# Kernel optimization log

Hardware: AMD Instinct MI355X
Metric: run time of the kernel (lower is better)

## Reference

```python
import jax, jax.numpy as jnp
import numpy as np

B, N, DIM = 2, 2048, 1024
HEADS, DIM_HEAD = 16, 64
INNER = HEADS * DIM_HEAD  # 1024
SCALE = DIM_HEAD ** -0.5


def setup_inputs() -> dict:
    key = jax.random.key(0)
    ks = jax.random.split(key, 8)
    s = DIM ** -0.5
    return {
        "x1": jax.random.normal(ks[0], (B, N, DIM), jnp.float32),
        "x2": jax.random.normal(ks[1], (B, N, DIM), jnp.float32),
        "W_qkv1": jax.random.normal(ks[2], (DIM, INNER * 3), jnp.float32) * s,
        "W_qkv2": jax.random.normal(ks[3], (DIM, INNER * 3), jnp.float32) * s,
        "W_out1": jax.random.normal(ks[4], (INNER, DIM), jnp.float32) * s,
        "b_out1": jnp.zeros((DIM,), jnp.float32),
        "W_out2": jax.random.normal(ks[5], (INNER, DIM), jnp.float32) * s,
        "b_out2": jnp.zeros((DIM,), jnp.float32),
    }


def _split_heads(t):
    # [b, n, (h d)] -> [b, h, n, d]
    b, n, _ = t.shape
    return t.reshape(b, n, HEADS, DIM_HEAD).transpose(0, 2, 1, 3)


def _merge_heads(t):
    # [b, h, n, d] -> [b, n, (h d)]
    b, h, n, d = t.shape
    return t.transpose(0, 2, 1, 3).reshape(b, n, h * d)


def reference(x1, x2, W_qkv1, W_qkv2, W_out1, b_out1, W_out2, b_out2):
    qkv1 = x1 @ W_qkv1  # [b, n, 3*inner]
    qkv2 = x2 @ W_qkv2
    q1, k1, v1 = [_split_heads(t) for t in jnp.split(qkv1, 3, axis=-1)]
    q2, k2, v2 = [_split_heads(t) for t in jnp.split(qkv2, 3, axis=-1)]

    # direction 1: queries from stream 2 attend to keys/values of stream 1
    dots1 = jnp.einsum('bhid,bhjd->bhij', q2, k1) * SCALE
    attn1 = jax.nn.softmax(dots1, axis=-1)
    out1 = jnp.einsum('bhij,bhjd->bhid', attn1, v1)
    out1 = _merge_heads(out1) @ W_out1 + b_out1

    # direction 2: queries from stream 1 attend to keys/values of stream 2
    dots2 = jnp.einsum('bhid,bhjd->bhij', q1, k2) * SCALE
    attn2 = jax.nn.softmax(dots2, axis=-1)
    out2 = jnp.einsum('bhij,bhjd->bhid', attn2, v2)
    out2 = _merge_heads(out2) @ W_out2 + b_out2

    return (out1, out2)
```

## Files before the change

### kernel.cpp

```cpp
#include <hip/hip_runtime.h>
#include <cmath>

typedef __attribute__((ext_vector_type(8))) short short8;
typedef __attribute__((ext_vector_type(4))) float f32x4;
typedef __attribute__((ext_vector_type(16))) float f32x16;
using u16 = unsigned short;

#define DEV static __device__ __forceinline__

DEV u16 f2bf(float f) {
  union { float f; unsigned u; } v; v.f = f;
  unsigned r = v.u + 0x7FFFu + ((v.u >> 16) & 1u);
  return (u16)(r >> 16);
}

DEV unsigned cvtpk(float lo, float hi_) {
  unsigned d;
  asm("v_cvt_pk_bf16_f32 %0, %1, %2" : "=v"(d) : "v"(lo), "v"(hi_));
  return d;
}

DEV void gld16(const void* g, void* l) {
  __builtin_amdgcn_global_load_lds(
      (const __attribute__((address_space(1))) unsigned*)g,
      (__attribute__((address_space(3))) unsigned*)l, 16, 0, 0);
}

__global__ void probe_scale(float* out) {
  if (threadIdx.x == 0 && blockIdx.x == 0) {
    float b = __builtin_amdgcn_exp2f(1.0f);
    out[0] = 0.125f / logf(b);
    out[1] = (fabsf(b - 2.0f) < 1e-3f) ? 0.0f : 1.0f;
  }
}

__global__ __launch_bounds__(256) void conv_f32_bf16(const float* __restrict__ s0,
                                                     const float* __restrict__ s1,
                                                     u16* __restrict__ d0,
                                                     u16* __restrict__ d1, int n8) {
  const float* src = blockIdx.z ? s1 : s0;
  u16* dst = blockIdx.z ? d1 : d0;
  int i = blockIdx.x * 256 + threadIdx.x;
  if (i >= n8) return;
  const float4* s = reinterpret_cast<const float4*>(src) + (size_t)i * 2;
  float4 a = s[0], b = s[1];
  union { u16 s[8]; uint4 v; } t;
  t.s[0]=f2bf(a.x); t.s[1]=f2bf(a.y); t.s[2]=f2bf(a.z); t.s[3]=f2bf(a.w);
  t.s[4]=f2bf(b.x); t.s[5]=f2bf(b.y); t.s[6]=f2bf(b.z); t.s[7]=f2bf(b.w);
  reinterpret_cast<uint4*>(dst)[i] = t.v;
}

__global__ __launch_bounds__(256) void transpose_w(const float* __restrict__ s0,
                                                   const float* __restrict__ s1,
                                                   u16* __restrict__ d0,
                                                   u16* __restrict__ d1, int R, int C,
                                                   int qcols,
                                                   const float* __restrict__ qscale_p) {
  const float* src = blockIdx.z ? s1 : s0;
  u16* dst = blockIdx.z ? d1 : d0;
  const float qscale = qscale_p ? qscale_p[0] : 1.0f;
  __shared__ float tile[32][33];
  int tx = threadIdx.x & 31, ty = threadIdx.x >> 5;
  int rb = blockIdx.y * 32, cb = blockIdx.x * 32;
#pragma unroll
  for (int j = 0; j < 32; j += 8)
    tile[ty + j][tx] = src[(size_t)(rb + ty + j) * C + cb + tx];
  __syncthreads();
#pragma unroll
  for (int j = 0; j < 32; j += 8) {
    int c = cb + ty + j;
    float sc = (c < qcols) ? qscale : 1.0f;
    dst[(size_t)c * R + rb + tx] = f2bf(tile[tx][ty + j] * sc);
  }
}

extern __shared__ char dsmem[];

__global__ __launch_bounds__(512, 2) void gemm256(
    const u16* __restrict__ A0, const u16* __restrict__ A1,
    const u16* __restrict__ B0, const u16* __restrict__ B1,
    u16* __restrict__ Q0, u16* __restrict__ Q1,
    u16* __restrict__ V0, u16* __restrict__ V1) {
  const int orig = blockIdx.x;
  const int wgid = (orig & 7) * 48 + (orig >> 3);
  const int z = wgid / 192, rr_ = wgid % 192;
  const int bx = rr_ / 12, by = rr_ % 12;
  const u16* Ag = z ? A1 : A0;
  const u16* Bg = z ? B1 : B0;
  const size_t m0 = (size_t)bx * 256, n0 = (size_t)by * 256;
  const int K = 1024;

  const int tid = threadIdx.x;
  const int lane = tid & 63;
  const int wave = tid >> 6;
  const int wm = wave >> 2, wn = wave & 3;
  const int lr = lane & 15, lk = lane >> 4;

  f32x4 acc[8][4] = {};

  auto STG = [&](int buf, int kt, int opi) {
    int idx = opi * 512 + tid;
    char* base = dsmem + buf * 65536;
    if (idx < 2048) {
      int r = idx >> 3, c = idx & 7;
      gld16(Ag + (m0 + r) * (size_t)K + kt * 64 + ((c ^ (r & 7)) * 8), base + idx * 16);
    } else {
      int j = idx - 2048;
      int r = j >> 3, c = j & 7;
      gld16(Bg + (n0 + r) * (size_t)K + kt * 64 + ((c ^ (r & 7)) * 8), base + 32768 + j * 16);
    }
  };
  auto DSA = [&](short8* af, int buf, int mg, int kh) {
#pragma unroll
    for (int i = 0; i < 4; ++i) {
      int row = wm * 128 + (mg * 4 + i) * 16 + lr;
      af[i] = *reinterpret_cast<const short8*>(
          dsmem + buf * 65536 + row * 128 + (((kh * 4 + lk) ^ (row & 7)) * 16));
    }
  };
  auto DSB = [&](short8* bf_, int buf, int kh) {
#pragma unroll
    for (int j = 0; j < 4; ++j) {
      int row = wn * 64 + j * 16 + lr;
      bf_[j] = *reinterpret_cast<const short8*>(
          dsmem + buf * 65536 + 32768 + row * 128 + (((kh * 4 + lk) ^ (row & 7)) * 16));
    }
  };

#pragma unroll
  for (int o = 0; o < 8; ++o) STG(0, 0, o);
  asm volatile("s_waitcnt vmcnt(0)" ::: "memory");
  __syncthreads();

  int cur = 0;
  for (int kt = 0; kt < 16; ++kt) {
    short8 af[4], bf_[4];
    const int more = (kt < 15);

    DSA(af, cur, 0, 0); DSB(bf_, cur, 0);
    if (more) { STG(cur ^ 1, kt + 1, 0); STG(cur ^ 1, kt + 1, 1);
                STG(cur ^ 1, kt + 1, 2); STG(cur ^ 1, kt + 1, 3); }
    __builtin_amdgcn_s_barrier();
    asm volatile("s_waitcnt lgkmcnt(0)" ::: "memory");
    __builtin_amdgcn_sched_barrier(0);
    __builtin_amdgcn_s_setprio(1);
#pragma unroll
    for (int i = 0; i < 4; ++i)
#pragma unroll
      for (int j = 0; j < 4; ++j)
        acc[i][j] = __builtin_amdgcn_mfma_f32_16x16x32_bf16(af[i], bf_[j], acc[i][j], 0, 0, 0);
    __builtin_amdgcn_s_setprio(0);
    __builtin_amdgcn_s_barrier();

    DSA(af, cur, 1, 0);
    if (more) { STG(cur ^ 1, kt + 1, 4); STG(cur ^ 1, kt + 1, 5);
                STG(cur ^ 1, kt + 1, 6); STG(cur ^ 1, kt + 1, 7); }
    __builtin_amdgcn_s_barrier();
    asm volatile("s_waitcnt lgkmcnt(0)" ::: "memory");
    __builtin_amdgcn_sched_barrier(0);
    __builtin_amdgcn_s_setprio(1);
#pragma unroll
    for (int i = 0; i < 4; ++i)
#pragma unroll
      for (int j = 0; j < 4; ++j)
        acc[4 + i][j] = __builtin_amdgcn_mfma_f32_16x16x32_bf16(af[i], bf_[j], acc[4 + i][j], 0, 0, 0);
    __builtin_amdgcn_s_setprio(0);
    __builtin_amdgcn_s_barrier();

    DSA(af, cur, 0, 1); DSB(bf_, cur, 1);
    __builtin_amdgcn_s_barrier();
    asm volatile("s_waitcnt lgkmcnt(0)" ::: "memory");
    __builtin_amdgcn_sched_barrier(0);
    __builtin_amdgcn_s_setprio(1);
#pragma unroll
    for (int i = 0; i < 4; ++i)
#pragma unroll
      for (int j = 0; j < 4; ++j)
        acc[i][j] = __builtin_amdgcn_mfma_f32_16x16x32_bf16(af[i], bf_[j], acc[i][j], 0, 0, 0);
    __builtin_amdgcn_s_setprio(0);
    __builtin_amdgcn_s_barrier();

    DSA(af, cur, 1, 1);
    __builtin_amdgcn_s_barrier();
    asm volatile("s_waitcnt lgkmcnt(0)" ::: "memory");
    __builtin_amdgcn_sched_barrier(0);
    __builtin_amdgcn_s_setprio(1);
#pragma unroll
    for (int i = 0; i < 4; ++i)
#pragma unroll
      for (int j = 0; j < 4; ++j)
        acc[4 + i][j] = __builtin_amdgcn_mfma_f32_16x16x32_bf16(af[i], bf_[j], acc[4 + i][j], 0, 0, 0);
    __builtin_amdgcn_s_setprio(0);
    asm volatile("s_waitcnt vmcnt(0)" ::: "memory");
    __builtin_amdgcn_s_barrier();
    cur ^= 1;
  }

  const int row0 = (int)m0 + wm * 128;
  const int col0 = (int)n0 + wn * 64;
  u16* Qo = z ? Q1 : Q0;
  u16* Vo = z ? V1 : V0;
  if (col0 < 2048) {
#pragma unroll
    for (int mf = 0; mf < 8; ++mf)
#pragma unroll
      for (int nf = 0; nf < 4; ++nf) {
        int col = col0 + nf * 16 + lr;
#pragma unroll
        for (int g = 0; g < 4; ++g) {
          int row = row0 + mf * 16 + lk * 4 + g;
          Qo[(size_t)row * 3072 + col] = f2bf(acc[mf][nf][g]);
        }
      }
  } else {
#pragma unroll
    for (int mf = 0; mf < 8; ++mf)
#pragma unroll
      for (int nf = 0; nf < 4; ++nf) {
        int col = col0 + nf * 16 + lr;
        int row = row0 + mf * 16 + lk * 4;
        size_t vbase = ((size_t)((row >> 11) * 1024 + (col - 2048))) * 2048 + (row & 2047);
        union { u16 s[4]; unsigned long long v; } pk;
#pragma unroll
        for (int g = 0; g < 4; ++g) pk.s[g] = f2bf(acc[mf][nf][g]);
        *reinterpret_cast<unsigned long long*>(Vo + vbase) = pk.v;
      }
  }
}

__global__ __launch_bounds__(256) void gemm_bt(
    const u16* __restrict__ A0, const u16* __restrict__ A1,
    const u16* __restrict__ B0, const u16* __restrict__ B1,
    float* __restrict__ Cf0, float* __restrict__ Cf1,
    const float* __restrict__ bias0, const float* __restrict__ bias1,
    int M, int N, int K) {
  const int z = blockIdx.z;
  const u16* A  = z ? A1 : A0;
  const u16* Bt = z ? B1 : B0;
  float* Cf = z ? Cf1 : Cf0;
  const float* bias = z ? bias1 : bias0;

  __shared__ __align__(16) char smem[32768];
  char* As = smem;
  char* Bs = smem + 16384;
  const int tid = threadIdx.x;
  const int lane = tid & 63, wave = tid >> 6;
  const int wm = wave >> 1, wn = wave & 1;
  const int lr = lane & 15, lk = lane >> 4;
  const size_t m0 = (size_t)blockIdx.x * 128, n0 = (size_t)blockIdx.y * 128;

  f32x4 acc[4][4] = {};

  for (int k0 = 0; k0 < K; k0 += 64) {
    __syncthreads();
#pragma unroll
    for (int i = 0; i < 4; ++i) {
      int idx = tid + i * 256;
      int r = idx >> 3, c = idx & 7;
      int cs = c ^ (r & 7);
      gld16(A + (m0 + r) * (size_t)K + k0 + cs * 8, As + idx * 16);
    }
#pragma unroll
    for (int i = 0; i < 4; ++i) {
      int idx = tid + i * 256;
      int r = idx >> 3, c = idx & 7;
      int cs = c ^ (r & 7);
      gld16(Bt + (n0 + r) * (size_t)K + k0 + cs * 8, Bs + idx * 16);
    }
    __syncthreads();
#pragma unroll
    for (int kk = 0; kk < 2; ++kk) {
      short8 af[4], bfr[4];
#pragma unroll
      for (int mf = 0; mf < 4; ++mf) {
        int r = wm * 64 + mf * 16 + lr;
        af[mf] = *reinterpret_cast<const short8*>(As + r * 128 + (((kk * 4 + lk) ^ (r & 7)) * 16));
      }
#pragma unroll
      for (int nf = 0; nf < 4; ++nf) {
        int r = wn * 64 + nf * 16 + lr;
        bfr[nf] = *reinterpret_cast<const short8*>(Bs + r * 128 + (((kk * 4 + lk) ^ (r & 7)) * 16));
      }
#pragma unroll
      for (int mf = 0; mf < 4; ++mf)
#pragma unroll
        for (int nf = 0; nf < 4; ++nf)
          acc[mf][nf] = __builtin_amdgcn_mfma_f32_16x16x32_bf16(af[mf], bfr[nf], acc[mf][nf], 0, 0, 0);
    }
  }
  const int row0 = (int)m0 + wm * 64, col0 = (int)n0 + wn * 64;
#pragma unroll
  for (int nf = 0; nf < 4; ++nf) {
    int col = col0 + nf * 16 + lr;
    float bv = bias[col];
#pragma unroll
    for (int mf = 0; mf < 4; ++mf)
#pragma unroll
      for (int g = 0; g < 4; ++g) {
        int row = row0 + mf * 16 + lk * 4 + g;
        Cf[(size_t)row * N + col] = acc[mf][nf][g] + bv;
      }
  }
}

#define KOFF0 0
#define VOFF0 (8192 + 64)
#define KOFF1 (16384 + 128)
#define VOFF1 (KOFF1 + 8192 + 64)

__global__ __launch_bounds__(256, 2) void flash(
    const u16* __restrict__ qkv1, const u16* __restrict__ qkv2,
    const u16* __restrict__ vT1, const u16* __restrict__ vT2,
    u16* __restrict__ ao1, u16* __restrict__ ao2,
    const float* __restrict__ sflag) {
  const int bid = blockIdx.x;
  const int bh_dir = bid & 63;
  const int qt = bid >> 6;
  const int dir = bh_dir >> 5;
  const int bh = bh_dir & 31;
  const int b = bh >> 4, h = bh & 15;
  const u16* qkvQ  = dir ? qkv1 : qkv2;
  const u16* qkvKV = dir ? qkv2 : qkv1;
  const u16* vT    = dir ? vT2 : vT1;
  u16* Oout        = dir ? ao2 : ao1;

  const bool nat = (sflag[1] != 0.0f);

  __shared__ __align__(16) char smem[33024];

  const int tid = threadIdx.x;
  const int lane = tid & 63, wave = tid >> 6;
  const int l31 = lane & 31, hi = lane >> 5;

  const int qbase = qt * 256 + wave * 64;
  const u16* qp0 = qkvQ + (size_t)(b * 2048 + qbase + l31) * 3072 + h * 64 + hi * 8;
  const u16* qp1 = qp0 + (size_t)32 * 3072;
  short8 qf0[4], qf1[4];
#pragma unroll
  for (int c = 0; c < 4; ++c) {
    qf0[c] = *reinterpret_cast<const short8*>(qp0 + c * 16);
    qf1[c] = *reinterpret_cast<const short8*>(qp1 + c * 16);
  }

  auto STAGE = [&](char* kb, char* vb, int kv0) {
#pragma unroll
    for (int i = 0; i < 2; ++i) {
      int idx = tid + i * 256;
      int r = idx >> 3, c = idx & 7, cs = c ^ (r & 7);
      gld16(qkvKV + (size_t)(b * 2048 + kv0 + r) * 3072 + 1024 + h * 64 + cs * 8, kb + idx * 16);
      gld16(vT + (size_t)(bh * 64 + r) * 2048 + kv0 + cs * 8, vb + idx * 16);
    }
  };

  auto EXPV = [&](f32x16& S) {
    if (nat) {
#pragma unroll
      for (int r = 0; r < 16; ++r) S[r] = __builtin_amdgcn_exp2f(S[r]);
    } else {
#pragma unroll
      for (int r = 0; r < 16; ++r) S[r] = __builtin_exp2f(S[r]);
    }
  };

  short8 ones;
#pragma unroll
  for (int j = 0; j < 8; ++j) ones[j] = (short)0x3F80;

  f32x16 oA0 = {}, oA1 = {}, oB0 = {}, oB1 = {}, laccA = {}, laccB = {};

  STAGE(smem + KOFF0, smem + VOFF0, 0);

  union U8 { unsigned u[4]; short8 s8; };

  for (int t = 0; t < 32; ++t) {
    char* Ks = smem + ((t & 1) ? KOFF1 : KOFF0);
    char* Vs = smem + ((t & 1) ? VOFF1 : VOFF0);
    __syncthreads();
    if (t < 31)
      STAGE(smem + ((t & 1) ? KOFF0 : KOFF1), smem + ((t & 1) ? VOFF0 : VOFF1), (t + 1) * 64);

    short8 kf[8];
#pragma unroll
    for (int c = 0; c < 4; ++c) {
      int sw = ((c * 2 + hi) ^ (l31 & 7)) * 16;
      kf[c]     = *reinterpret_cast<const short8*>(Ks + l31 * 128 + sw);
      kf[c + 4] = *reinterpret_cast<const short8*>(Ks + (32 + l31) * 128 + sw);
    }

    f32x16 sA0 = {}, sA1 = {};
#pragma unroll
    for (int c = 0; c < 4; ++c) {
      sA0 = __builtin_amdgcn_mfma_f32_32x32x16_bf16(kf[c],     qf0[c], sA0, 0, 0, 0);
      sA1 = __builtin_amdgcn_mfma_f32_32x32x16_bf16(kf[c + 4], qf0[c], sA1, 0, 0, 0);
    }
    EXPV(sA0); EXPV(sA1);
    short8 paA[4];
#pragma unroll
    for (int kc = 0; kc < 4; ++kc) {
      const f32x16& S = (kc < 2) ? sA0 : sA1;
      int rb = (kc & 1) * 8;
      unsigned a0 = cvtpk(S[rb + 0], S[rb + 1]);
      unsigned b0 = cvtpk(S[rb + 4], S[rb + 5]);
      asm volatile("v_permlane32_swap_b32 %0, %1" : "+v"(a0), "+v"(b0));
      unsigned a1 = cvtpk(S[rb + 2], S[rb + 3]);
      unsigned b1 = cvtpk(S[rb + 6], S[rb + 7]);
      asm volatile("v_permlane32_swap_b32 %0, %1" : "+v"(a1), "+v"(b1));
      U8 u; u.u[0] = a0; u.u[1] = a1; u.u[2] = b0; u.u[3] = b1;
      paA[kc] = u.s8;
    }

    f32x16 sB0 = {}, sB1 = {};
#pragma unroll
    for (int c = 0; c < 4; ++c) {
      sB0 = __builtin_amdgcn_mfma_f32_32x32x16_bf16(kf[c],     qf1[c], sB0, 0, 0, 0);
      sB1 = __builtin_amdgcn_mfma_f32_32x32x16_bf16(kf[c + 4], qf1[c], sB1, 0, 0, 0);
    }

    short8 vf[8];
#pragma unroll
    for (int kc = 0; kc < 4; ++kc) {
      int sw = ((kc * 2 + hi) ^ (l31 & 7)) * 16;
      vf[kc]     = *reinterpret_cast<const short8*>(Vs + l31 * 128 + sw);
      vf[kc + 4] = *reinterpret_cast<const short8*>(Vs + (32 + l31) * 128 + sw);
    }

    EXPV(sB0); EXPV(sB1);
    short8 paB[4];
#pragma unroll
    for (int kc = 0; kc < 4; ++kc) {
      const f32x16& S = (kc < 2) ? sB0 : sB1;
      int rb = (kc & 1) * 8;
      unsigned a0 = cvtpk(S[rb + 0], S[rb + 1]);
      unsigned b0 = cvtpk(S[rb + 4], S[rb + 5]);
      asm volatile("v_permlane32_swap_b32 %0, %1" : "+v"(a0), "+v"(b0));
      unsigned a1 = cvtpk(S[rb + 2], S[rb + 3]);
      unsigned b1 = cvtpk(S[rb + 6], S[rb + 7]);
      asm volatile("v_permlane32_swap_b32 %0, %1" : "+v"(a1), "+v"(b1));
      U8 u; u.u[0] = a0; u.u[1] = a1; u.u[2] = b0; u.u[3] = b1;
      paB[kc] = u.s8;
    }

#pragma unroll
    for (int kc = 0; kc < 4; ++kc) {
      oA0 = __builtin_amdgcn_mfma_f32_32x32x16_bf16(paA[kc], vf[kc],     oA0, 0, 0, 0);
      oA1 = __builtin_amdgcn_mfma_f32_32x32x16_bf16(paA[kc], vf[kc + 4], oA1, 0, 0, 0);
      oB0 = __builtin_amdgcn_mfma_f32_32x32x16_bf16(paB[kc], vf[kc],     oB0, 0, 0, 0);
      oB1 = __builtin_amdgcn_mfma_f32_32x32x16_bf16(paB[kc], vf[kc + 4], oB1, 0, 0, 0);
      laccA = __builtin_amdgcn_mfma_f32_32x32x16_bf16(paA[kc], ones, laccA, 0, 0, 0);
      laccB = __builtin_amdgcn_mfma_f32_32x32x16_bf16(paB[kc], ones, laccB, 0, 0, 0);
    }
  }

  const int rowbase = b * 2048 + qt * 256 + wave * 64;
#pragma unroll
  for (int r = 0; r < 16; ++r) {
    int q = (r & 3) + 8 * (r >> 2) + 4 * hi;
    float liA = 1.0f / laccA[r], liB = 1.0f / laccB[r];
    u16* opA = Oout + (size_t)(rowbase + q) * 1024 + h * 64 + l31;
    u16* opB = opA + (size_t)32 * 1024;
    opA[0]  = f2bf(oA0[r] * liA);
    opA[32] = f2bf(oA1[r] * liA);
    opB[0]  = f2bf(oB0[r] * liB);
    opB[32] = f2bf(oB1[r] * liB);
  }
}

extern "C" void kernel_launch(void* const* d_in, const int* in_sizes, int n_in,
                              void* d_out, int out_size, void* d_ws, size_t ws_size,
                              hipStream_t stream) {
  const float* x1  = (const float*)d_in[0];
  const float* x2  = (const float*)d_in[1];
  const float* Wq1 = (const float*)d_in[2];
  const float* Wq2 = (const float*)d_in[3];
  const float* Wo1 = (const float*)d_in[4];
  const float* bo1 = (const float*)d_in[5];
  const float* Wo2 = (const float*)d_in[6];
  const float* bo2 = (const float*)d_in[7];
  float* out = (float*)d_out;

  char* ws = (char*)d_ws;
  u16* x1b  = (u16*)(ws + 0);
  u16* x2b  = (u16*)(ws + 8388608);
  u16* Wq1t = (u16*)(ws + 16777216);
  u16* Wq2t = (u16*)(ws + 23068672);
  u16* Wo1t = (u16*)(ws + 29360128);
  u16* Wo2t = (u16*)(ws + 31457280);
  u16* qkv1 = (u16*)(ws + 33554432);
  u16* qkv2 = (u16*)(ws + 58720256);
  u16* vT1  = (u16*)(ws + 83886080);
  u16* vT2  = (u16*)(ws + 92274688);
  u16* ao1  = (u16*)(ws + 100663296);
  u16* ao2  = (u16*)(ws + 109051904);

  float* scale_buf = (float*)(qkv1 + 2048);

  hipFuncSetAttribute(reinterpret_cast<const void*>(gemm256),
                      hipFuncAttributeMaxDynamicSharedMemorySize, 131072);

  probe_scale<<<dim3(1), 64, 0, stream>>>(scale_buf);

  conv_f32_bf16<<<dim3(2048, 1, 2), 256, 0, stream>>>(x1, x2, x1b, x2b, 4194304 / 8);
  transpose_w<<<dim3(96, 32, 2), 256, 0, stream>>>(Wq1, Wq2, Wq1t, Wq2t, 1024, 3072,
                                                   1024, scale_buf);
  transpose_w<<<dim3(32, 32, 2), 256, 0, stream>>>(Wo1, Wo2, Wo1t, Wo2t, 1024, 1024,
                                                   0, nullptr);

  gemm256<<<dim3(384), 512, 131072, stream>>>(x1b, x2b, Wq1t, Wq2t,
                                              qkv1, qkv2, vT1, vT2);

  flash<<<dim3(512), 256, 0, stream>>>(qkv1, qkv2, vT1, vT2, ao1, ao2, scale_buf);

  gemm_bt<<<dim3(32, 8, 2), 256, 0, stream>>>(ao1, ao2, Wo1t, Wo2t,
                                              out, out + 4194304, bo1, bo2,
                                              4096, 1024, 1024);
}
```

Baseline: 214.5 us.

## Shrink QKV GEMM tile to 256x128 and use inline-asm hardware exp

The QKV projection GEMM now uses 256x128 output tiles with a 4x2 wave grid instead of 256x256. That doubles the grid to 768 workgroups and lowers LDS use to 96KB per block, so more blocks are resident and the 304 CUs are loaded more evenly. The cost is less data reuse per tile and more global traffic for the A operand. Separately, the flash kernel's exp now calls v_exp_f32 through inline asm, and the probe kernel checks its accuracy more carefully and falls back to the natural-exp scale if the check fails. The asm volatile exp may also limit how the compiler schedules the exp instructions.

```diff
diff --git a/kernel.cpp b/kernel.cpp
--- a/kernel.cpp
+++ b/kernel.cpp
@@ -26,11 +26,29 @@
       (__attribute__((address_space(3))) unsigned*)l, 16, 0, 0);
 }
 
+DEV float hw_exp(float x) {
+  float y;
+  asm volatile("v_exp_f32 %0, %1\n\ts_nop 1" : "=v"(y) : "v"(x));
+  return y;
+}
+
 __global__ void probe_scale(float* out) {
   if (threadIdx.x == 0 && blockIdx.x == 0) {
-    float b = __builtin_amdgcn_exp2f(1.0f);
-    out[0] = 0.125f / logf(b);
-    out[1] = (fabsf(b - 2.0f) < 1e-3f) ? 0.0f : 1.0f;
+    float one;
+    asm volatile("v_mov_b32 %0, 1.0" : "=v"(one));
+    float b = hw_exp(one);
+    float lnb = logf(b);
+    bool ok = (fabsf(b - 2.0f) < 0.25f) && (lnb > 0.1f);
+    const float xs[3] = {0.3333f, -5.7f, 9.1f};
+    for (int i = 0; i < 3; ++i) {
+      float xo;
+      asm volatile("v_mov_b32 %0, %1" : "=v"(xo) : "v"(xs[i]));
+      float yn = hw_exp(xo);
+      float yr = expf(lnb * xs[i]);
+      ok = ok && (fabsf(yn - yr) <= 2e-4f * fabsf(yr));
+    }
+    out[0] = ok ? (0.125f / lnb) : (0.125f / 0.69314718056f);
+    out[1] = ok ? 1.0f : 0.0f;
   }
 }
 
@@ -82,25 +100,25 @@
     u16* __restrict__ Q0, u16* __restrict__ Q1,
     u16* __restrict__ V0, u16* __restrict__ V1) {
   const int orig = blockIdx.x;
-  const int wgid = (orig & 7) * 48 + (orig >> 3);
-  const int z = wgid / 192, rr_ = wgid % 192;
-  const int bx = rr_ / 12, by = rr_ % 12;
+  const int wgid = (orig & 7) * 96 + (orig >> 3);
+  const int z = wgid / 384, rr_ = wgid % 384;
+  const int bx = rr_ / 24, by = rr_ % 24;
   const u16* Ag = z ? A1 : A0;
   const u16* Bg = z ? B1 : B0;
-  const size_t m0 = (size_t)bx * 256, n0 = (size_t)by * 256;
+  const size_t m0 = (size_t)bx * 256, n0 = (size_t)by * 128;
   const int K = 1024;
 
   const int tid = threadIdx.x;
   const int lane = tid & 63;
   const int wave = tid >> 6;
-  const int wm = wave >> 2, wn = wave & 3;
+  const int wm = wave >> 1, wn = wave & 1;
   const int lr = lane & 15, lk = lane >> 4;
 
-  f32x4 acc[8][4] = {};
+  f32x4 acc[4][4] = {};
 
   auto STG = [&](int buf, int kt, int opi) {
     int idx = opi * 512 + tid;
-    char* base = dsmem + buf * 65536;
+    char* base = dsmem + buf * 49152;
     if (idx < 2048) {
       int r = idx >> 3, c = idx & 7;
       gld16(Ag + (m0 + r) * (size_t)K + kt * 64 + ((c ^ (r & 7)) * 8), base + idx * 16);
@@ -110,12 +128,12 @@
       gld16(Bg + (n0 + r) * (size_t)K + kt * 64 + ((c ^ (r & 7)) * 8), base + 32768 + j * 16);
     }
   };
-  auto DSA = [&](short8* af, int buf, int mg, int kh) {
+  auto DSA = [&](short8* af, int buf, int kh) {
 #pragma unroll
     for (int i = 0; i < 4; ++i) {
-      int row = wm * 128 + (mg * 4 + i) * 16 + lr;
+      int row = wm * 64 + i * 16 + lr;
       af[i] = *reinterpret_cast<const short8*>(
-          dsmem + buf * 65536 + row * 128 + (((kh * 4 + lk) ^ (row & 7)) * 16));
+          dsmem + buf * 49152 + row * 128 + (((kh * 4 + lk) ^ (row & 7)) * 16));
     }
   };
   auto DSB = [&](short8* bf_, int buf, int kh) {
@@ -123,12 +141,12 @@
     for (int j = 0; j < 4; ++j) {
       int row = wn * 64 + j * 16 + lr;
       bf_[j] = *reinterpret_cast<const short8*>(
-          dsmem + buf * 65536 + 32768 + row * 128 + (((kh * 4 + lk) ^ (row & 7)) * 16));
+          dsmem + buf * 49152 + 32768 + row * 128 + (((kh * 4 + lk) ^ (row & 7)) * 16));
     }
   };
 
 #pragma unroll
-  for (int o = 0; o < 8; ++o) STG(0, 0, o);
+  for (int o = 0; o < 6; ++o) STG(0, 0, o);
   asm volatile("s_waitcnt vmcnt(0)" ::: "memory");
   __syncthreads();
 
@@ -137,9 +155,9 @@
     short8 af[4], bf_[4];
     const int more = (kt < 15);
 
-    DSA(af, cur, 0, 0); DSB(bf_, cur, 0);
-    if (more) { STG(cur ^ 1, kt + 1, 0); STG(cur ^ 1, kt + 1, 1);
-                STG(cur ^ 1, kt + 1, 2); STG(cur ^ 1, kt + 1, 3); }
+    DSA(af, cur, 0); DSB(bf_, cur, 0);
+    if (more) { STG(cur ^ 1, kt + 1, 0); STG(cur ^ 1, kt + 1, 1); STG(cur ^ 1, kt + 1, 2);
+                STG(cur ^ 1, kt + 1, 3); STG(cur ^ 1, kt + 1, 4); STG(cur ^ 1, kt + 1, 5); }
     __builtin_amdgcn_s_barrier();
     asm volatile("s_waitcnt lgkmcnt(0)" ::: "memory");
     __builtin_amdgcn_sched_barrier(0);
@@ -152,9 +170,7 @@
     __builtin_amdgcn_s_setprio(0);
     __builtin_amdgcn_s_barrier();
 
-    DSA(af, cur, 1, 0);
-    if (more) { STG(cur ^ 1, kt + 1, 4); STG(cur ^ 1, kt + 1, 5);
-                STG(cur ^ 1, kt + 1, 6); STG(cur ^ 1, kt + 1, 7); }
+    DSA(af, cur, 1); DSB(bf_, cur, 1);
     __builtin_amdgcn_s_barrier();
     asm volatile("s_waitcnt lgkmcnt(0)" ::: "memory");
     __builtin_amdgcn_sched_barrier(0);
@@ -163,46 +179,20 @@
     for (int i = 0; i < 4; ++i)
 #pragma unroll
       for (int j = 0; j < 4; ++j)
-        acc[4 + i][j] = __builtin_amdgcn_mfma_f32_16x16x32_bf16(af[i], bf_[j], acc[4 + i][j], 0, 0, 0);
-    __builtin_amdgcn_s_setprio(0);
-    __builtin_amdgcn_s_barrier();
-
-    DSA(af, cur, 0, 1); DSB(bf_, cur, 1);
-    __builtin_amdgcn_s_barrier();
-    asm volatile("s_waitcnt lgkmcnt(0)" ::: "memory");
-    __builtin_amdgcn_sched_barrier(0);
-    __builtin_amdgcn_s_setprio(1);
-#pragma unroll
-    for (int i = 0; i < 4; ++i)
-#pragma unroll
-      for (int j = 0; j < 4; ++j)
         acc[i][j] = __builtin_amdgcn_mfma_f32_16x16x32_bf16(af[i], bf_[j], acc[i][j], 0, 0, 0);
-    __builtin_amdgcn_s_setprio(0);
-    __builtin_amdgcn_s_barrier();
-
-    DSA(af, cur, 1, 1);
-    __builtin_amdgcn_s_barrier();
-    asm volatile("s_waitcnt lgkmcnt(0)" ::: "memory");
-    __builtin_amdgcn_sched_barrier(0);
-    __builtin_amdgcn_s_setprio(1);
-#pragma unroll
-    for (int i = 0; i < 4; ++i)
-#pragma unroll
-      for (int j = 0; j < 4; ++j)
-        acc[4 + i][j] = __builtin_amdgcn_mfma_f32_16x16x32_bf16(af[i], bf_[j], acc[4 + i][j], 0, 0, 0);
     __builtin_amdgcn_s_setprio(0);
     asm volatile("s_waitcnt vmcnt(0)" ::: "memory");
     __builtin_amdgcn_s_barrier();
     cur ^= 1;
   }
 
-  const int row0 = (int)m0 + wm * 128;
+  const int row0 = (int)m0 + wm * 64;
   const int col0 = (int)n0 + wn * 64;
   u16* Qo = z ? Q1 : Q0;
   u16* Vo = z ? V1 : V0;
   if (col0 < 2048) {
 #pragma unroll
-    for (int mf = 0; mf < 8; ++mf)
+    for (int mf = 0; mf < 4; ++mf)
 #pragma unroll
       for (int nf = 0; nf < 4; ++nf) {
         int col = col0 + nf * 16 + lr;
@@ -214,7 +204,7 @@
       }
   } else {
 #pragma unroll
-    for (int mf = 0; mf < 8; ++mf)
+    for (int mf = 0; mf < 4; ++mf)
 #pragma unroll
       for (int nf = 0; nf < 4; ++nf) {
         int col = col0 + nf * 16 + lr;
@@ -355,7 +345,7 @@
   auto EXPV = [&](f32x16& S) {
     if (nat) {
 #pragma unroll
-      for (int r = 0; r < 16; ++r) S[r] = __builtin_amdgcn_exp2f(S[r]);
+      for (int r = 0; r < 16; ++r) S[r] = hw_exp(S[r]);
     } else {
 #pragma unroll
       for (int r = 0; r < 16; ++r) S[r] = __builtin_exp2f(S[r]);
@@ -495,7 +485,7 @@
   float* scale_buf = (float*)(qkv1 + 2048);
 
   hipFuncSetAttribute(reinterpret_cast<const void*>(gemm256),
-                      hipFuncAttributeMaxDynamicSharedMemorySize, 131072);
+                      hipFuncAttributeMaxDynamicSharedMemorySize, 98304);
 
   probe_scale<<<dim3(1), 64, 0, stream>>>(scale_buf);
 
@@ -505,8 +495,8 @@
   transpose_w<<<dim3(32, 32, 2), 256, 0, stream>>>(Wo1, Wo2, Wo1t, Wo2t, 1024, 1024,
                                                    0, nullptr);
 
-  gemm256<<<dim3(384), 512, 131072, stream>>>(x1b, x2b, Wq1t, Wq2t,
-                                              qkv1, qkv2, vT1, vT2);
+  gemm256<<<dim3(768), 512, 98304, stream>>>(x1b, x2b, Wq1t, Wq2t,
+                                             qkv1, qkv2, vT1, vT2);
 
   flash<<<dim3(512), 256, 0, stream>>>(qkv1, qkv2, vT1, vT2, ao1, ao2, scale_buf);
 
```

Result: faster. 190.8 us (-11.1%).
